# Kernel optimization log

Measured on AMD Instinct MI355X. Metric: run time of the kernel, lower is better.

Reference implementation:

```python
import jax, jax.numpy as jnp
import numpy as np

B, M, D, OUT = 16384, 4096, 512, 128


def setup_inputs() -> dict:
    key = jax.random.key(0)
    ks = jax.random.split(key, 5)
    x = jax.random.normal(ks[0], (B, D), dtype=jnp.float32)
    support = jax.random.normal(ks[1], (M, D), dtype=jnp.float32)
    gamma = jnp.float32(1.0)
    head_w = jax.random.normal(ks[2], (OUT, M), dtype=jnp.float32) / np.sqrt(M)
    head_b = jax.random.normal(ks[3], (OUT,), dtype=jnp.float32) * 0.01
    scale = jnp.ones((1,), dtype=jnp.float32)
    shift = jnp.zeros((1,), dtype=jnp.float32)
    return {"x": x, "support": support, "gamma": gamma,
            "head_w": head_w, "head_b": head_b,
            "scale": scale, "shift": shift}


def reference(x, support, gamma, head_w, head_b, scale, shift):
    x2 = jnp.sum(x * x, axis=-1, keepdims=True)           # [B, 1]
    s2 = jnp.sum(support * support, axis=-1)              # [M]
    xs = jnp.einsum('bd,md->bm', x, support)              # [B, M]
    sqdist = jnp.maximum(x2 + s2[None, :] - 2.0 * xs, 0.0)
    k = jnp.exp(-gamma * sqdist)                          # RBF kernel [B, M]
    out = jnp.einsum('bm,om->bo', k, head_w) + head_b     # linear head [B, OUT]
    return scale * out + shift
```

## Files before the change

kernel.cpp:

```cpp
#include <hip/hip_runtime.h>

typedef unsigned int u32;
typedef unsigned short u16;
typedef unsigned char u8;
typedef __attribute__((ext_vector_type(8))) __bf16 bf16x8;
typedef __attribute__((ext_vector_type(4))) float f32x4;

#define NB 16384
#define NM 4096
#define ND 512
#define NOUT 128
#define L2E 1.44269504088896340736f


__device__ __forceinline__ u16 f2bf(float f) {
  u32 u = __float_as_uint(f);
  u += 0x7FFFu + ((u >> 16) & 1u);
  return (u16)(u >> 16);
}

__device__ __forceinline__ u8 f2fp8(float f) {
  u32 u = __float_as_uint(f);
  u32 s = (u >> 24) & 0x80u;
  u32 au = u & 0x7FFFFFFFu;
  if (au < 0x3C800000u) return (u8)s;
  au += 0x000FFFFFu + ((au >> 20) & 1u);
  u32 e = (au >> 23) - 120u;
  u32 m = (au >> 20) & 7u;
  return (u8)(s | (e << 3) | m);
}

__device__ __forceinline__ void stage16(const void* g, void* l) {
  __builtin_amdgcn_global_load_lds((__attribute__((address_space(1))) void*)g,
                                   (__attribute__((address_space(3))) void*)l,
                                   16, 0, 0);
}

__device__ __forceinline__ uint4 pack8bf(float4 v0, float4 v1) {
  uint4 pk;
  pk.x = (u32)f2bf(v0.x) | ((u32)f2bf(v0.y) << 16);
  pk.y = (u32)f2bf(v0.z) | ((u32)f2bf(v0.w) << 16);
  pk.z = (u32)f2bf(v1.x) | ((u32)f2bf(v1.y) << 16);
  pk.w = (u32)f2bf(v1.z) | ((u32)f2bf(v1.w) << 16);
  return pk;
}

__device__ __forceinline__ uint2 pack8f8(float4 v0, float4 v1) {
  uint2 pk;
  pk.x = (u32)f2fp8(v0.x) | ((u32)f2fp8(v0.y) << 8) |
         ((u32)f2fp8(v0.z) << 16) | ((u32)f2fp8(v0.w) << 24);
  pk.y = (u32)f2fp8(v1.x) | ((u32)f2fp8(v1.y) << 8) |
         ((u32)f2fp8(v1.z) << 16) | ((u32)f2fp8(v1.w) << 24);
  return pk;
}

__global__ __launch_bounds__(256) void prep_all(const float* __restrict__ x,
                                                const float* __restrict__ s,
                                                const float* __restrict__ hw,
                                                const float* __restrict__ gamma_p,
                                                u8*  __restrict__ x_ws,
                                                u8*  __restrict__ s_ws,
                                                u16* __restrict__ hw_ws,
                                                float* __restrict__ x2g,
                                                float* __restrict__ s2g,
                                                float* __restrict__ out) {
  __shared__ uint2 t8[2048];
  __shared__ uint4 t16[2048];
  const int tid = threadIdx.x, bid = blockIdx.x;
  const int lane = tid & 63, w = tid >> 6;

  if (bid < 640) {
    const bool isx = bid < 512;
    const int blk = isx ? bid : (bid - 512);
    const float* src_m = isx ? x : s;
    u8*    dst_ws = isx ? x_ws : s_ws;
    float* sq_out = isx ? x2g : s2g;
    const float gl   = gamma_p[0] * L2E;
    const float cmul = isx ? 1.0f : (-2.0f * gl);
    const int big  = isx ? (blk >> 1) : (blk >> 2);
    const int roff = isx ? ((blk & 1) * 32) : ((blk & 3) * 32);
    const int rows = isx ? 64 : 128;

    #pragma unroll
    for (int p = 0; p < 8; ++p) {
      const int row = p * 4 + w;
      const float* src = src_m + (size_t)(blk * 32 + row) * ND + lane * 8;
      float4 v0 = *(const float4*)src;
      float4 v1 = *(const float4*)(src + 4);
      float ss = v0.x*v0.x + v0.y*v0.y + v0.z*v0.z + v0.w*v0.w
               + v1.x*v1.x + v1.y*v1.y + v1.z*v1.z + v1.w*v1.w;
      #pragma unroll
      for (int off = 32; off > 0; off >>= 1) ss += __shfl_down(ss, off);
      if (lane == 0) sq_out[blk * 32 + row] = gl * ss;
      v0.x *= cmul; v0.y *= cmul; v0.z *= cmul; v0.w *= cmul;
      v1.x *= cmul; v1.y *= cmul; v1.z *= cmul; v1.w *= cmul;
      t8[lane * 32 + ((row + lane) & 31)] = pack8f8(v0, v1);
    }
    __syncthreads();
    #pragma unroll
    for (int p = 0; p < 8; ++p) {
      const int kg = p * 8 + (tid >> 5);
      const int row = tid & 31;
      uint2 pk = t8[kg * 32 + ((row + kg) & 31)];
      *(uint2*)&dst_ws[(((size_t)(big * 64 + kg)) * rows + roff + row) * 8] = pk;
    }
  } else if (bid < 672) {
    const int blk = bid - 640;
    #pragma unroll
    for (int p = 0; p < 8; ++p) {
      const int o = p * 16 + (tid >> 4);
      const int kg = tid & 15;
      const float* src = hw + (size_t)o * NM + blk * 128 + kg * 8;
      float4 v0 = *(const float4*)src;
      float4 v1 = *(const float4*)(src + 4);
      t16[o * 16 + ((kg + o) & 15)] = pack8bf(v0, v1);
    }
    __syncthreads();
    #pragma unroll
    for (int it = 0; it < 8; ++it) {
      const int kg = it * 2 + (tid >> 7);
      const int o = tid & 127;
      uint4 pk = t16[o * 16 + ((kg + o) & 15)];
      *(uint4*)&hw_ws[(((size_t)(blk * 16 + kg)) * 128 + o) * 8] = pk;
    }
  } else {
    float4* o4 = (float4*)out;
    const float4 z = {0.f, 0.f, 0.f, 0.f};
    size_t base = (size_t)(bid - 672) * 32768 + tid;
    #pragma unroll 8
    for (int i = 0; i < 128; ++i) o4[base + (size_t)i * 256] = z;
  }
}

__global__ __launch_bounds__(256, 2)
void rbf_fused(const u8* __restrict__ x_ws, const u8* __restrict__ s_ws,
               const u16* __restrict__ hw_ws, const float* __restrict__ x2g,
               const float* __restrict__ s2g, const float* __restrict__ head_b,
               const float* __restrict__ scale_p, const float* __restrict__ shift_p,
               float* __restrict__ out)
{
  __shared__ __align__(16) char smem[65536];

  const int tid  = threadIdx.x;
  const int w    = tid >> 6;
  const int lane = tid & 63;
  const int quad = lane >> 4;
  const int l16  = lane & 15;
  const int wr   = w & 1;
  const int wc   = w >> 1;
  const int xcd  = blockIdx.x & 7;
  const int rb   = (blockIdx.x >> 3) * 2 + (xcd & 1);
  const int half = xcd >> 1;
  const int b0   = rb * 64;

  const float vscale = scale_p[0];
  const float vshift = shift_p[0];

  const u8* xsrc = x_ws + (size_t)rb * 32768;
  const u8* ssrc = s_ws + (size_t)(half * 8) * 65536;

  #pragma unroll
  for (int i = 0; i < 8; ++i)
    stage16(xsrc + i * 4096 + tid * 16, smem + i * 4096 + tid * 16);

  f32x4 x2v[2];
  #pragma unroll
  for (int r = 0; r < 2; ++r)
    x2v[r] = *(const f32x4*)&x2g[b0 + wr * 32 + r * 16 + quad * 4];

  const f32x4 zf = {0.f, 0.f, 0.f, 0.f};
  f32x4 acc_xs[2][4];
  f32x4 acc_out[2][4];
  #pragma unroll
  for (int r = 0; r < 2; ++r)
    #pragma unroll
    for (int c = 0; c < 4; ++c) { acc_xs[r][c] = zf; acc_out[r][c] = zf; }

  auto stage_sgrp = [&](int mt, int grp, int buf) {
    const u8* sp = ssrc + (size_t)mt * 65536 + grp * 8192;
    char* dp = smem + 32768 + buf * 8192;
    stage16(sp + tid * 16, dp + tid * 16);
    stage16(sp + 4096 + tid * 16, dp + 4096 + tid * 16);
  };

  auto compute_kc = [&](int kc, int kcL, int buf) {
    long long a[2], b[4];
    #pragma unroll
    for (int r = 0; r < 2; ++r)
      a[r] = *(const long long*)(smem + ((kc * 4 + quad) * 64 + wr * 32 + r * 16 + l16) * 8);
    #pragma unroll
    for (int c = 0; c < 4; ++c)
      b[c] = *(const long long*)(smem + 32768 + buf * 8192 +
                                 ((kcL * 4 + quad) * 128 + wc * 64 + c * 16 + l16) * 8);
    #pragma unroll
    for (int r = 0; r < 2; ++r)
      #pragma unroll
      for (int c = 0; c < 4; ++c)
        acc_xs[r][c] = __builtin_amdgcn_mfma_f32_16x16x32_fp8_fp8(a[r], b[c], acc_xs[r][c], 0, 0, 0);
  };

  auto gemm2_step = [&](int mtg2, int ks) {
    const int kg = ks * 4 + quad;
    bf16x8 a2[2], b2[4];
    #pragma unroll
    for (int r = 0; r < 2; ++r)
      a2[r] = *(const bf16x8*)(smem + 49152 + (kg * 64 + wr * 32 + r * 16 + l16) * 16);
    const size_t slab = (size_t)(mtg2 * 16 + kg);
    #pragma unroll
    for (int c = 0; c < 4; ++c)
      b2[c] = *(const bf16x8*)(hw_ws + (slab * 128 + wc * 64 + c * 16 + l16) * 8);
    #pragma unroll
    for (int r = 0; r < 2; ++r)
      #pragma unroll
      for (int c = 0; c < 4; ++c)
        acc_out[r][c] = __builtin_amdgcn_mfma_f32_16x16x32_bf16(a2[r], b2[c], acc_out[r][c], 0, 0, 0);
  };

  stage_sgrp(0, 0, 0);
  __syncthreads();

  #pragma unroll 1
  for (int mt = 0; mt < 8; ++mt) {
    const int mtg = half * 8 + mt;
    #pragma unroll
    for (int grp = 0; grp < 8; ++grp) {
      if (grp < 7)      stage_sgrp(mt, grp + 1, (grp + 1) & 1);
      else if (mt < 7)  stage_sgrp(mt + 1, 0, 0);
      compute_kc(grp * 2,     0, grp & 1);
      compute_kc(grp * 2 + 1, 1, grp & 1);
      if (mt > 0 && (grp & 1) == 0) gemm2_step(mtg - 1, grp >> 1);
      if (grp < 7) __syncthreads();
    }

    {
      float s2v[4];
      #pragma unroll
      for (int c = 0; c < 4; ++c)
        s2v[c] = s2g[mtg * 128 + wc * 64 + c * 16 + l16];
      #pragma unroll
      for (int r = 0; r < 2; ++r)
        #pragma unroll
        for (int c = 0; c < 4; ++c) {
          const int cl = wc * 64 + c * 16 + l16;
          char* kbase = smem + 49152 + (cl >> 3) * 1024 + (cl & 7) * 2;
          #pragma unroll
          for (int i = 0; i < 4; ++i) {
            const int row = wr * 32 + r * 16 + quad * 4 + i;
            const float t = acc_xs[r][c][i] + x2v[r][i] + s2v[c];
            float kv = __builtin_amdgcn_exp2f(-t);
            kv = fminf(kv, 1.0f);
            *(u16*)(kbase + row * 16) = (u16)(__float_as_uint(kv) >> 16);
            acc_xs[r][c][i] = 0.0f;
          }
        }
    }
    __syncthreads();
  }

  #pragma unroll
  for (int ks = 0; ks < 4; ++ks)
    gemm2_step(half * 8 + 7, ks);

  float addv[4];
  #pragma unroll
  for (int c = 0; c < 4; ++c) {
    const int col = wc * 64 + c * 16 + l16;
    addv[c] = (half == 0) ? (vscale * head_b[col] + vshift) : 0.0f;
  }
  #pragma unroll
  for (int r = 0; r < 2; ++r)
    #pragma unroll
    for (int c = 0; c < 4; ++c) {
      const int col = wc * 64 + c * 16 + l16;
      #pragma unroll
      for (int i = 0; i < 4; ++i) {
        const int row = b0 + wr * 32 + r * 16 + quad * 4 + i;
        atomicAdd(&out[(size_t)row * NOUT + col], vscale * acc_out[r][c][i] + addv[c]);
      }
    }
}

extern "C" void kernel_launch(void* const* d_in, const int* in_sizes, int n_in,
                              void* d_out, int out_size, void* d_ws, size_t ws_size,
                              hipStream_t stream) {
  const float* x       = (const float*)d_in[0];
  const float* support = (const float*)d_in[1];
  const float* gamma   = (const float*)d_in[2];
  const float* head_w  = (const float*)d_in[3];
  const float* head_b  = (const float*)d_in[4];
  const float* scale   = (const float*)d_in[5];
  const float* shift   = (const float*)d_in[6];
  float* out = (float*)d_out;

  char* w = (char*)d_ws;
  u8*    x_ws  = (u8*)(w);
  u8*    s_ws  = (u8*)(w + 8388608);
  u16*   hw_ws = (u16*)(w + 10485760);
  float* x2g   = (float*)(w + 11534336);
  float* s2g   = (float*)(w + 11599872);

  prep_all<<<688, 256, 0, stream>>>(x, support, head_w, gamma,
                                    x_ws, s_ws, hw_ws, x2g, s2g, out);
  rbf_fused<<<1024, 256, 0, stream>>>(x_ws, s_ws, hw_ws, x2g, s2g,
                                      head_b, scale, shift, out);
}
```

Before: 192.6 us.

## Replace syncthreads with explicit vmcnt waits and prefetch head weights early

Replaces the __syncthreads calls in the fused RBF kernel with raw s_barrier plus hand-counted s_waitcnt vmcnt values. Global loads of the head-weight fragments are now issued before the support-tile staging, so they overlap with it instead of stalling inside the second GEMM. The s2 loads are hoisted to the top of each M tile. The zero-fill of the output is spread over more prep blocks with less work each. Hand-tuned vmcnt counts are fragile: if the real number of outstanding loads differs from what was assumed, the kernel can read data that has not arrived yet.

```diff
diff --git a/kernel.cpp b/kernel.cpp
--- a/kernel.cpp
+++ b/kernel.cpp
@@ -12,6 +12,9 @@
 #define NOUT 128
 #define L2E 1.44269504088896340736f
 
+
+#define WAITVM(N) do { asm volatile("s_waitcnt vmcnt(" #N ")" ::: "memory"); \
+                       __builtin_amdgcn_sched_barrier(0); } while (0)
 
 __device__ __forceinline__ u16 f2bf(float f) {
   u32 u = __float_as_uint(f);
@@ -126,9 +129,9 @@
   } else {
     float4* o4 = (float4*)out;
     const float4 z = {0.f, 0.f, 0.f, 0.f};
-    size_t base = (size_t)(bid - 672) * 32768 + tid;
+    size_t base = (size_t)(bid - 672) * 8192 + tid;
     #pragma unroll 8
-    for (int i = 0; i < 128; ++i) o4[base + (size_t)i * 256] = z;
+    for (int i = 0; i < 32; ++i) o4[base + (size_t)i * 256] = z;
   }
 }
 
@@ -199,16 +202,20 @@
         acc_xs[r][c] = __builtin_amdgcn_mfma_f32_16x16x32_fp8_fp8(a[r], b[c], acc_xs[r][c], 0, 0, 0);
   };
 
-  auto gemm2_step = [&](int mtg2, int ks) {
+  auto g2_load = [&](int mtg2, int ks, bf16x8* b2) {
     const int kg = ks * 4 + quad;
-    bf16x8 a2[2], b2[4];
+    const size_t slab = (size_t)(mtg2 * 16 + kg);
+    #pragma unroll
+    for (int c = 0; c < 4; ++c)
+      b2[c] = *(const bf16x8*)(hw_ws + (slab * 128 + wc * 64 + c * 16 + l16) * 8);
+  };
+
+  auto gemm2_mma = [&](int ks, const bf16x8* b2) {
+    const int kg = ks * 4 + quad;
+    bf16x8 a2[2];
     #pragma unroll
     for (int r = 0; r < 2; ++r)
       a2[r] = *(const bf16x8*)(smem + 49152 + (kg * 64 + wr * 32 + r * 16 + l16) * 16);
-    const size_t slab = (size_t)(mtg2 * 16 + kg);
-    #pragma unroll
-    for (int c = 0; c < 4; ++c)
-      b2[c] = *(const bf16x8*)(hw_ws + (slab * 128 + wc * 64 + c * 16 + l16) * 8);
     #pragma unroll
     for (int r = 0; r < 2; ++r)
       #pragma unroll
@@ -221,22 +228,36 @@
 
   #pragma unroll 1
   for (int mt = 0; mt < 8; ++mt) {
-    const int mtg = half * 8 + mt;
+    const int mtg  = half * 8 + mt;
+    const int mtg2 = mtg - (mt > 0);
+
+    float s2v[4];
+    #pragma unroll
+    for (int c = 0; c < 4; ++c)
+      s2v[c] = s2g[mtg * 128 + wc * 64 + c * 16 + l16];
+
     #pragma unroll
     for (int grp = 0; grp < 8; ++grp) {
+      if (grp > 0) __builtin_amdgcn_s_barrier();
+
+      bf16x8 b2[4];
+      if ((grp & 1) == 0) g2_load(mtg2, grp >> 1, b2);
+
       if (grp < 7)      stage_sgrp(mt, grp + 1, (grp + 1) & 1);
       else if (mt < 7)  stage_sgrp(mt + 1, 0, 0);
+
+      if (grp == 0)            WAITVM(10);
+      else if (grp == 7)       { if (mt < 7) { WAITVM(2); } else { WAITVM(0); } }
+      else if ((grp & 1) == 0) WAITVM(6);
+      else                     WAITVM(2);
+      __builtin_amdgcn_s_barrier();
+
       compute_kc(grp * 2,     0, grp & 1);
       compute_kc(grp * 2 + 1, 1, grp & 1);
-      if (mt > 0 && (grp & 1) == 0) gemm2_step(mtg - 1, grp >> 1);
-      if (grp < 7) __syncthreads();
+      if (mt > 0 && (grp & 1) == 0) gemm2_mma(grp >> 1, b2);
     }
 
     {
-      float s2v[4];
-      #pragma unroll
-      for (int c = 0; c < 4; ++c)
-        s2v[c] = s2g[mtg * 128 + wc * 64 + c * 16 + l16];
       #pragma unroll
       for (int r = 0; r < 2; ++r)
         #pragma unroll
@@ -254,12 +275,17 @@
           }
         }
     }
-    __syncthreads();
+    asm volatile("s_waitcnt lgkmcnt(0)" ::: "memory");
+    __builtin_amdgcn_sched_barrier(0);
+    __builtin_amdgcn_s_barrier();
   }
 
   #pragma unroll
-  for (int ks = 0; ks < 4; ++ks)
-    gemm2_step(half * 8 + 7, ks);
+  for (int ks = 0; ks < 4; ++ks) {
+    bf16x8 b2[4];
+    g2_load(half * 8 + 7, ks, b2);
+    gemm2_mma(ks, b2);
+  }
 
   float addv[4];
   #pragma unroll
@@ -299,7 +325,7 @@
   float* x2g   = (float*)(w + 11534336);
   float* s2g   = (float*)(w + 11599872);
 
-  prep_all<<<688, 256, 0, stream>>>(x, support, head_w, gamma,
+  prep_all<<<736, 256, 0, stream>>>(x, support, head_w, gamma,
                                     x_ws, s_ws, hw_ws, x2g, s2g, out);
   rbf_fused<<<1024, 256, 0, stream>>>(x_ws, s_ws, hw_ws, x2g, s2g,
                                       head_b, scale, shift, out);
```

Result: no change. 192.8 us (+0.1%).
